# Kernel tuning notes

Hardware: AMD Instinct MI355X
Metric: run time of the kernel (lower is better)

The kernel has to match this reference:

```python
import jax, jax.numpy as jnp
import numpy as np

B, NR_BOX, D = 512, 18, 2048
NR_OBJ = NR_BOX - 2
K = 3
NUM_CLASSES = 174
NUM_CAT = 321


def setup_inputs() -> dict:
    key = jax.random.key(0)
    k1, k2, k3, k4, k5, k6 = jax.random.split(key, 6)
    obj_fea = jax.random.normal(k1, (B, NR_BOX, D), dtype=jnp.float32)
    # cooccurrence: nonnegative, sparse-ish, first (pad) column zero as in the torch code
    cooc = jax.random.uniform(k2, (NUM_CLASSES, NUM_CAT), dtype=jnp.float32)
    mask = jax.random.uniform(k3, (NUM_CLASSES, NUM_CAT)) < 0.5
    cooc = jnp.where(mask, cooc, 0.0).at[:, 0].set(0.0)
    obj_indicator = jax.random.randint(k4, (B, NR_BOX), 0, 2).astype(jnp.int32)
    obj_category = jax.random.randint(k5, (B, NR_BOX), 0, NUM_CAT).astype(jnp.int32)
    labels = jax.random.randint(k6, (B,), 0, NUM_CLASSES).astype(jnp.int32)
    return {
        'obj_fea': obj_fea,
        'cooccurrence': cooc,
        'obj_indicator': obj_indicator,
        'obj_category': obj_category,
        'labels': labels,
    }


def reference(obj_fea, cooccurrence, obj_indicator, obj_category, labels):
    Bn, nr_box, d = obj_fea.shape
    nr_obj = nr_box - 2
    ind = obj_indicator[:, 2:]          # (B, nr_obj)
    cats = obj_category[:, 2:]          # (B, nr_obj)
    ori_comp = obj_fea.mean(axis=1)     # (B, d)
    objs = obj_fea[:, 2:]               # (B, nr_obj, d), hands dropped
    label_onehot = jax.nn.one_hot(labels, NUM_CLASSES, dtype=obj_fea.dtype)  # (B, C)

    # W[i, b, j] = cooccurrence[labels[i], cats[b, j]]  (candidate weights per sample i)
    cooc_lab = cooccurrence[labels]                 # (B, NUM_CAT)
    W = cooc_lab[:, cats]                           # (B, B, nr_obj)
    eye = jnp.eye(Bn, dtype=bool)
    W = jnp.where(eye[:, :, None], 0.0, W)          # exclude own video (cand_obj[i] = 0)
    Wf = W.reshape(Bn, Bn * nr_obj)

    # softmax(log w) over nonzero support == w / sum(w); sample via categorical on log-weights
    logits = jnp.where(Wf > 0, jnp.log(jnp.where(Wf > 0, Wf, 1.0)), -jnp.inf)
    has_cand = (Wf > 0).any(axis=1) & (ind != 0).any(axis=1)  # (B,)

    rng = jax.random.key(42)
    r1, r2, r3 = jax.random.split(rng, 3)
    sel = jax.random.categorical(r1, logits, shape=(K, Bn)).T   # (B, K) flat candidate ids
    batch_idx = sel // nr_obj
    box_idx = sel % nr_obj
    sel_fea = objs[batch_idx, box_idx]              # (B, K, d)
    sel_label = label_onehot[batch_idx]             # (B, K, C)

    lam = jax.random.uniform(r2, (Bn, 1, 1), dtype=obj_fea.dtype)  # Beta(1,1)==U(0,1), one per sample
    slots = jax.random.randint(r3, (Bn, K), 0, nr_obj)
    own_fea = jnp.take_along_axis(objs, slots[:, :, None], axis=1)  # (B, K, d)

    mixed_fea = own_fea * lam + sel_fea * (1.0 - lam)
    mixed_label = label_onehot[:, None, :] * lam + sel_label * (1.0 - lam)

    # fallback path: mean of own objects + own one-hot label, repeated K times
    fb_fea = jnp.broadcast_to(objs.mean(axis=1)[:, None, :], mixed_fea.shape)
    fb_label = jnp.broadcast_to(label_onehot[:, None, :], mixed_label.shape)
    m = has_cand[:, None, None]
    mix_fea = jnp.where(m, mixed_fea, fb_fea)
    mix_label = jnp.where(m, mixed_label, fb_label)
    return ori_comp, mix_fea, mix_label
```

## Files before the change

### kernel.cpp

```cpp
#include <hip/hip_runtime.h>
#include <stdint.h>
#include <math.h>

#define NBOX 18
#define BB 512
#define DD 2048
#define NOBJ 16
#define KK 3
#define NCLS 174
#define NCAT 321
#define NQ 4
#define QCAND 2048
#define NPART 16

__host__ __device__ __forceinline__ uint32_t rotl32(uint32_t x, int d) {
  return (x << d) | (x >> (32 - d));
}

__host__ __device__ __forceinline__ void threefry2x32(uint32_t k0, uint32_t k1,
                                                      uint32_t x0, uint32_t x1,
                                                      uint32_t& o0, uint32_t& o1) {
  uint32_t ks2 = k0 ^ k1 ^ 0x1BD11BDAu;
  x0 += k0; x1 += k1;
#define TFR(r) x0 += x1; x1 = rotl32(x1, r); x1 ^= x0;
#define R4A TFR(13) TFR(15) TFR(26) TFR(6)
#define R4B TFR(17) TFR(29) TFR(16) TFR(24)
  R4A x0 += k1;  x1 += ks2 + 1u;
  R4B x0 += ks2; x1 += k0 + 2u;
  R4A x0 += k0;  x1 += k1 + 3u;
  R4B x0 += k1;  x1 += ks2 + 4u;
  R4A x0 += ks2; x1 += k0 + 5u;
#undef R4A
#undef R4B
#undef TFR
  o0 = x0; o1 = x1;
}

__device__ __forceinline__ float bits_to_unit(uint32_t bits) {
  float f = __uint_as_float((bits >> 9) | 0x3f800000u);
  return f - 1.0f;
}

__global__ __launch_bounds__(256) void sample_kernel(
    const float* __restrict__ cooc, const int* __restrict__ obj_cat,
    const int* __restrict__ labels, uint32_t r1h, uint32_t r1l,
    unsigned long long* __restrict__ part, int* __restrict__ cnts) {
  const int gb = blockIdx.x;
  const int b = gb >> 2;
  const int q = gb & 3;
  const int tid = threadIdx.x;
  const int lane = tid & 63;
  const int wid = tid >> 6;

  __shared__ unsigned short jl[QCAND];
  __shared__ float wl[QCAND];

  const int lab = labels[b];
  const float* crow = cooc + (size_t)lab * NCAT;
  const int seg = wid << 9;
  const int jbase = (q << 11) + seg;

  int cnt = 0;
#pragma unroll 1
  for (int c = 0; c < 8; ++c) {
    int j = jbase + (c << 6) + lane;
    int jb = j >> 4;
    float w = 0.0f;
    if (jb != b) w = crow[obj_cat[jb * NBOX + 2 + (j & 15)]];
    unsigned long long m = __ballot(w > 0.0f);
    if (w > 0.0f) {
      int rank = __popcll(m & ((1ull << lane) - 1ull));
      jl[seg + cnt + rank] = (unsigned short)j;
      wl[seg + cnt + rank] = w;
    }
    cnt += __popcll(m);
  }

  const uint32_t cbase0 = ((uint32_t)b) << 13;
  const uint32_t kstep = 1u << 22;
  float bw0 = 0.f, bt0 = 1.f, bw1 = 0.f, bt1 = 1.f, bw2 = 0.f, bt2 = 1.f;
  int bj0 = 0, bj1 = 0, bj2 = 0;
#pragma unroll 1
  for (int p = lane; p < cnt; p += 64) {
    uint32_t j = jl[seg + p];
    float w = wl[seg + p];
    uint32_t cc = cbase0 + j;
    uint32_t x0, x1, y0, y1, z0, z1;
    threefry2x32(r1h, r1l, 0u, cc, x0, x1);
    threefry2x32(r1h, r1l, 0u, cc + kstep, y0, y1);
    threefry2x32(r1h, r1l, 0u, cc + 2u * kstep, z0, z1);
    float t0 = -__log2f(fmaxf(bits_to_unit(x0 ^ x1), 1.1920929e-07f));
    float t1 = -__log2f(fmaxf(bits_to_unit(y0 ^ y1), 1.1920929e-07f));
    float t2 = -__log2f(fmaxf(bits_to_unit(z0 ^ z1), 1.1920929e-07f));
    if (w * bt0 > bw0 * t0) { bw0 = w; bt0 = t0; bj0 = (int)j; }
    if (w * bt1 > bw1 * t1) { bw1 = w; bt1 = t1; bj1 = (int)j; }
    if (w * bt2 > bw2 * t2) { bw2 = w; bt2 = t2; bj2 = (int)j; }
  }
#pragma unroll
  for (int mm = 1; mm < 64; mm <<= 1) {
    float ow, ot; int oj;
    ow = __shfl_xor(bw0, mm, 64); ot = __shfl_xor(bt0, mm, 64); oj = __shfl_xor(bj0, mm, 64);
    { float l = ow * bt0, r = bw0 * ot;
      if (l > r || (l == r && oj < bj0)) { bw0 = ow; bt0 = ot; bj0 = oj; } }
    ow = __shfl_xor(bw1, mm, 64); ot = __shfl_xor(bt1, mm, 64); oj = __shfl_xor(bj1, mm, 64);
    { float l = ow * bt1, r = bw1 * ot;
      if (l > r || (l == r && oj < bj1)) { bw1 = ow; bt1 = ot; bj1 = oj; } }
    ow = __shfl_xor(bw2, mm, 64); ot = __shfl_xor(bt2, mm, 64); oj = __shfl_xor(bj2, mm, 64);
    { float l = ow * bt2, r = bw2 * ot;
      if (l > r || (l == r && oj < bj2)) { bw2 = ow; bt2 = ot; bj2 = oj; } }
  }
  if (lane == 0) {
    const int pw = q * 4 + wid;
    const size_t pb = (size_t)b * KK * NPART;
    part[pb + 0 * NPART + pw] =
        ((unsigned long long)__float_as_uint(bw0 / bt0) << 32) | (uint32_t)(8192 - bj0);
    part[pb + 1 * NPART + pw] =
        ((unsigned long long)__float_as_uint(bw1 / bt1) << 32) | (uint32_t)(8192 - bj1);
    part[pb + 2 * NPART + pw] =
        ((unsigned long long)__float_as_uint(bw2 / bt2) << 32) | (uint32_t)(8192 - bj2);
    cnts[b * NPART + pw] = cnt;
  }
}

__global__ __launch_bounds__(256) void stream_mix_kernel(
    const float* __restrict__ obj_fea, const int* __restrict__ obj_ind,
    const int* __restrict__ labels,
    const unsigned long long* __restrict__ part, const int* __restrict__ cnts,
    uint32_t r2h, uint32_t r2l, uint32_t r3bh, uint32_t r3bl,
    float* __restrict__ ori, float* __restrict__ mixf, float* __restrict__ mixl) {
  const int bx = blockIdx.x;
  const int b = bx >> 1;
  const int h = bx & 1;
  const int tid = threadIdx.x;
  const int off = (h << 8) + tid;

  __shared__ int s_sel[KK];
  __shared__ int s_slots[KK];
  __shared__ float s_lam;
  __shared__ int s_hc;

  if (tid < KK) {
    const int k = tid;
    const unsigned long long* pp = part + ((size_t)b * KK + k) * NPART;
    unsigned long long best = pp[0];
#pragma unroll
    for (int p = 1; p < NPART; ++p) {
      unsigned long long v = pp[p];
      if (v > best) best = v;
    }
    s_sel[k] = 8192 - (int)(best & 0xFFFFFFFFull);
    uint32_t s0, s1;
    threefry2x32(r3bh, r3bl, 0u, (uint32_t)(b * KK + k), s0, s1);
    s_slots[k] = (int)((s0 ^ s1) & 15u);
  } else if (tid == 3) {
    int tot = 0;
#pragma unroll
    for (int p = 0; p < NPART; ++p) tot += cnts[b * NPART + p];
    int any = 0;
#pragma unroll
    for (int o = 0; o < NOBJ; ++o) any |= (obj_ind[b * NBOX + 2 + o] != 0);
    s_hc = (tot > 0) && any;
  } else if (tid == 4) {
    uint32_t c0, c1;
    threefry2x32(r2h, r2l, 0u, (uint32_t)b, c0, c1);
    s_lam = bits_to_unit(c0 ^ c1);
  }

  const float4* fea4 = (const float4*)obj_fea;
  const size_t rb = (size_t)b * NBOX * 512 + off;
  float4 v0 = fea4[rb];
  float4 v1 = fea4[rb + 512];
  float4 S = make_float4(v0.x + v1.x, v0.y + v1.y, v0.z + v1.z, v0.w + v1.w);
#pragma unroll
  for (int r = 2; r < NBOX; ++r) {
    float4 a = fea4[rb + (size_t)r * 512];
    S.x += a.x; S.y += a.y; S.z += a.z; S.w += a.w;
  }
  {
    const float is = 1.0f / 18.0f;
    ((float4*)ori)[(size_t)b * 512 + off] =
        make_float4(S.x * is, S.y * is, S.z * is, S.w * is);
  }
  float4 S16 = make_float4(S.x - v0.x - v1.x, S.y - v0.y - v1.y,
                           S.z - v0.z - v1.z, S.w - v0.w - v1.w);
  __syncthreads();

  const int hc = s_hc;
  const float l = s_lam, l1 = 1.0f - l;
  float4* mixf4 = (float4*)mixf;
  if (hc) {
#pragma unroll 1
    for (int k = 0; k < KK; ++k) {
      int s = s_sel[k];
      int bi = s >> 4, bo = s & 15, sl = s_slots[k];
      float4 a = fea4[((size_t)b * NBOX + 2 + sl) * 512 + off];
      float4 e = fea4[((size_t)bi * NBOX + 2 + bo) * 512 + off];
      float4 o;
      o.x = a.x * l + e.x * l1; o.y = a.y * l + e.y * l1;
      o.z = a.z * l + e.z * l1; o.w = a.w * l + e.w * l1;
      mixf4[((size_t)b * KK + k) * 512 + off] = o;
    }
  } else {
    const float is = 1.0f / 16.0f;
    float4 o = make_float4(S16.x * is, S16.y * is, S16.z * is, S16.w * is);
#pragma unroll
    for (int k = 0; k < KK; ++k) mixf4[((size_t)b * KK + k) * 512 + off] = o;
  }

  if (h == 0 && tid < NCLS) {
    int lb = labels[b];
#pragma unroll 1
    for (int k = 0; k < KK; ++k) {
      float val;
      if (hc) {
        int ls = labels[s_sel[k] >> 4];
        val = (tid == lb ? l : 0.0f) + (tid == ls ? l1 : 0.0f);
      } else {
        val = (tid == lb) ? 1.0f : 0.0f;
      }
      mixl[(size_t)(b * KK + k) * NCLS + tid] = val;
    }
  }
}

extern "C" void kernel_launch(void* const* d_in, const int* in_sizes, int n_in,
                              void* d_out, int out_size, void* d_ws, size_t ws_size,
                              hipStream_t stream) {
  (void)in_sizes; (void)n_in; (void)out_size; (void)ws_size;
  const float* obj_fea = (const float*)d_in[0];
  const float* cooc    = (const float*)d_in[1];
  const int* obj_ind   = (const int*)d_in[2];
  const int* obj_cat   = (const int*)d_in[3];
  const int* labels    = (const int*)d_in[4];

  float* out  = (float*)d_out;
  float* ori  = out;
  float* mixf = out + (size_t)BB * DD;
  float* mixl = mixf + (size_t)BB * KK * DD;

  char* ws = (char*)d_ws;
  unsigned long long* part = (unsigned long long*)ws;
  int* cnts = (int*)(ws + (size_t)BB * KK * NPART * 8);

  uint32_t r1h, r1l, r2h, r2l, r3h, r3l;
  threefry2x32(0u, 42u, 0u, 0u, r1h, r1l);
  threefry2x32(0u, 42u, 0u, 1u, r2h, r2l);
  threefry2x32(0u, 42u, 0u, 2u, r3h, r3l);
  uint32_t r3bh, r3bl;
  threefry2x32(r3h, r3l, 0u, 1u, r3bh, r3bl);

  hipLaunchKernelGGL(sample_kernel, dim3(BB * NQ), dim3(256), 0, stream,
                     cooc, obj_cat, labels, r1h, r1l, part, cnts);
  hipLaunchKernelGGL(stream_mix_kernel, dim3(BB * 2), dim3(256), 0, stream,
                     obj_fea, obj_ind, labels, part, cnts,
                     r2h, r2l, r3bh, r3bl, ori, mixf, mixl);
}
```

Baseline: 46.41 us.

## Fuse feature-mean streaming into sampling kernel via async global-to-LDS loads

The full obj_fea streaming (mean over 18 boxes for ori and the 16-object fallback mean) moves from the mix kernel into the sampling kernel. There it is issued as asynchronous global_load_lds transfers that overlap the threefry-based categorical sampling. The sampling grid grows from 4 to 16 slices per sample, giving 64 partial winners. The mix kernel reduces those with a wave shuffle and reads the precomputed fallback mean from workspace. This aims to hide the bandwidth-bound reduction behind the compute-bound RNG work, at the cost of extra workspace traffic and more partials to combine.

After: 52.41 us. +12.9%, slower.

```diff
diff --git a/kernel.cpp b/kernel.cpp
--- a/kernel.cpp
+++ b/kernel.cpp
@@ -9,9 +9,9 @@
 #define KK 3
 #define NCLS 174
 #define NCAT 321
-#define NQ 4
-#define QCAND 2048
-#define NPART 16
+#define NSL 16
+#define SCAND 512
+#define NPART 64
 
 __host__ __device__ __forceinline__ uint32_t rotl32(uint32_t x, int d) {
   return (x << d) | (x >> (32 - d));
@@ -41,28 +41,47 @@
   return f - 1.0f;
 }
 
-__global__ __launch_bounds__(256) void sample_kernel(
-    const float* __restrict__ cooc, const int* __restrict__ obj_cat,
-    const int* __restrict__ labels, uint32_t r1h, uint32_t r1l,
-    unsigned long long* __restrict__ part, int* __restrict__ cnts) {
+__device__ __forceinline__ void gload_lds16(const void* g, void* l) {
+  __builtin_amdgcn_global_load_lds(
+      (const __attribute__((address_space(1))) unsigned int*)g,
+      (__attribute__((address_space(3))) unsigned int*)l, 16, 0, 0);
+}
+
+__global__ __launch_bounds__(256) void sample_stream_kernel(
+    const float* __restrict__ obj_fea, const float* __restrict__ cooc,
+    const int* __restrict__ obj_cat, const int* __restrict__ labels,
+    uint32_t r1h, uint32_t r1l,
+    unsigned long long* __restrict__ part, int* __restrict__ cnts,
+    float* __restrict__ ori, float4* __restrict__ m16ws) {
   const int gb = blockIdx.x;
-  const int b = gb >> 2;
-  const int q = gb & 3;
+  const int b = gb >> 4;
+  const int o = gb & 15;
   const int tid = threadIdx.x;
   const int lane = tid & 63;
   const int wid = tid >> 6;
 
-  __shared__ unsigned short jl[QCAND];
-  __shared__ float wl[QCAND];
+  __shared__ float4 slds[NBOX * 32];
+  __shared__ unsigned short jl[SCAND];
+  __shared__ float wl[SCAND];
+
+  const int col0 = o << 5;
+  const float4* fea4 = (const float4*)obj_fea;
+  {
+    const float4* gbase = fea4 + (size_t)b * NBOX * 512 + col0;
+    for (int i = wid; i < 9; i += 4) {
+      const float4* g = gbase + (size_t)(2 * i + (lane >> 5)) * 512 + (lane & 31);
+      gload_lds16((const void*)g, (void*)((char*)slds + i * 1024));
+    }
+  }
+  __builtin_amdgcn_sched_barrier(0);
 
   const int lab = labels[b];
   const float* crow = cooc + (size_t)lab * NCAT;
-  const int seg = wid << 9;
-  const int jbase = (q << 11) + seg;
-
+  const int seg = wid << 7;
+  const int jbase = (o << 9) + seg;
   int cnt = 0;
 #pragma unroll 1
-  for (int c = 0; c < 8; ++c) {
+  for (int c = 0; c < 2; ++c) {
     int j = jbase + (c << 6) + lane;
     int jb = j >> 4;
     float w = 0.0f;
@@ -100,17 +119,17 @@
   for (int mm = 1; mm < 64; mm <<= 1) {
     float ow, ot; int oj;
     ow = __shfl_xor(bw0, mm, 64); ot = __shfl_xor(bt0, mm, 64); oj = __shfl_xor(bj0, mm, 64);
-    { float l = ow * bt0, r = bw0 * ot;
-      if (l > r || (l == r && oj < bj0)) { bw0 = ow; bt0 = ot; bj0 = oj; } }
+    { float lv = ow * bt0, rv = bw0 * ot;
+      if (lv > rv || (lv == rv && oj < bj0)) { bw0 = ow; bt0 = ot; bj0 = oj; } }
     ow = __shfl_xor(bw1, mm, 64); ot = __shfl_xor(bt1, mm, 64); oj = __shfl_xor(bj1, mm, 64);
-    { float l = ow * bt1, r = bw1 * ot;
-      if (l > r || (l == r && oj < bj1)) { bw1 = ow; bt1 = ot; bj1 = oj; } }
+    { float lv = ow * bt1, rv = bw1 * ot;
+      if (lv > rv || (lv == rv && oj < bj1)) { bw1 = ow; bt1 = ot; bj1 = oj; } }
     ow = __shfl_xor(bw2, mm, 64); ot = __shfl_xor(bt2, mm, 64); oj = __shfl_xor(bj2, mm, 64);
-    { float l = ow * bt2, r = bw2 * ot;
-      if (l > r || (l == r && oj < bj2)) { bw2 = ow; bt2 = ot; bj2 = oj; } }
+    { float lv = ow * bt2, rv = bw2 * ot;
+      if (lv > rv || (lv == rv && oj < bj2)) { bw2 = ow; bt2 = ot; bj2 = oj; } }
   }
   if (lane == 0) {
-    const int pw = q * 4 + wid;
+    const int pw = (o << 2) + wid;
     const size_t pb = (size_t)b * KK * NPART;
     part[pb + 0 * NPART + pw] =
         ((unsigned long long)__float_as_uint(bw0 / bt0) << 32) | (uint32_t)(8192 - bj0);
@@ -120,14 +139,41 @@
         ((unsigned long long)__float_as_uint(bw2 / bt2) << 32) | (uint32_t)(8192 - bj2);
     cnts[b * NPART + pw] = cnt;
   }
-}
-
-__global__ __launch_bounds__(256) void stream_mix_kernel(
+
+  __syncthreads();
+  if (wid == 0) {
+    const int col = lane & 31;
+    const int rh = lane >> 5;
+    float4 acc = make_float4(0.f, 0.f, 0.f, 0.f);
+    float4 v0 = acc, v1 = acc;
+#pragma unroll
+    for (int r = 0; r < 9; ++r) {
+      float4 t = slds[(rh * 9 + r) * 32 + col];
+      if (r == 0) v0 = t;
+      if (r == 1) v1 = t;
+      acc.x += t.x; acc.y += t.y; acc.z += t.z; acc.w += t.w;
+    }
+    float4 oth;
+    oth.x = __shfl_xor(acc.x, 32, 64); oth.y = __shfl_xor(acc.y, 32, 64);
+    oth.z = __shfl_xor(acc.z, 32, 64); oth.w = __shfl_xor(acc.w, 32, 64);
+    if (rh == 0) {
+      float4 S = make_float4(acc.x + oth.x, acc.y + oth.y, acc.z + oth.z, acc.w + oth.w);
+      const float i18 = 1.0f / 18.0f, i16 = 1.0f / 16.0f;
+      const size_t oidx = (size_t)b * 512 + col0 + col;
+      ((float4*)ori)[oidx] = make_float4(S.x * i18, S.y * i18, S.z * i18, S.w * i18);
+      m16ws[oidx] = make_float4((S.x - v0.x - v1.x) * i16, (S.y - v0.y - v1.y) * i16,
+                                (S.z - v0.z - v1.z) * i16, (S.w - v0.w - v1.w) * i16);
+    }
+  }
+}
+
+__global__ __launch_bounds__(256) void mix_kernel(
     const float* __restrict__ obj_fea, const int* __restrict__ obj_ind,
     const int* __restrict__ labels,
     const unsigned long long* __restrict__ part, const int* __restrict__ cnts,
+    const float4* __restrict__ m16ws,
     uint32_t r2h, uint32_t r2l, uint32_t r3bh, uint32_t r3bl,
-    float* __restrict__ ori, float* __restrict__ mixf, float* __restrict__ mixl) {
+    float* __restrict__ mixf, float* __restrict__ mixl) {
   const int bx = blockIdx.x;
   const int b = bx >> 1;
   const int h = bx & 1;
@@ -137,56 +183,48 @@
   __shared__ int s_sel[KK];
   __shared__ int s_slots[KK];
   __shared__ float s_lam;
-  __shared__ int s_hc;
-
-  if (tid < KK) {
-    const int k = tid;
-    const unsigned long long* pp = part + ((size_t)b * KK + k) * NPART;
-    unsigned long long best = pp[0];
-#pragma unroll
-    for (int p = 1; p < NPART; ++p) {
-      unsigned long long v = pp[p];
-      if (v > best) best = v;
-    }
-    s_sel[k] = 8192 - (int)(best & 0xFFFFFFFFull);
+  __shared__ int s_cnt;
+  __shared__ int s_any;
+
+  if (tid < 64) {
+    unsigned long long p0 = part[((size_t)b * KK + 0) * NPART + tid];
+    unsigned long long p1 = part[((size_t)b * KK + 1) * NPART + tid];
+    unsigned long long p2 = part[((size_t)b * KK + 2) * NPART + tid];
+    int ct = cnts[b * NPART + tid];
+#pragma unroll
+    for (int mm = 1; mm < 64; mm <<= 1) {
+      unsigned long long q;
+      q = __shfl_xor(p0, mm, 64); if (q > p0) p0 = q;
+      q = __shfl_xor(p1, mm, 64); if (q > p1) p1 = q;
+      q = __shfl_xor(p2, mm, 64); if (q > p2) p2 = q;
+      ct |= __shfl_xor(ct, mm, 64);
+    }
+    if (tid == 0) {
+      s_sel[0] = 8192 - (int)(p0 & 0xFFFFFFFFull);
+      s_sel[1] = 8192 - (int)(p1 & 0xFFFFFFFFull);
+      s_sel[2] = 8192 - (int)(p2 & 0xFFFFFFFFull);
+      s_cnt = ct;
+    }
+  } else if (tid < 67) {
+    const int k = tid - 64;
     uint32_t s0, s1;
     threefry2x32(r3bh, r3bl, 0u, (uint32_t)(b * KK + k), s0, s1);
     s_slots[k] = (int)((s0 ^ s1) & 15u);
-  } else if (tid == 3) {
-    int tot = 0;
-#pragma unroll
-    for (int p = 0; p < NPART; ++p) tot += cnts[b * NPART + p];
-    int any = 0;
-#pragma unroll
-    for (int o = 0; o < NOBJ; ++o) any |= (obj_ind[b * NBOX + 2 + o] != 0);
-    s_hc = (tot > 0) && any;
-  } else if (tid == 4) {
+  } else if (tid == 67) {
     uint32_t c0, c1;
     threefry2x32(r2h, r2l, 0u, (uint32_t)b, c0, c1);
     s_lam = bits_to_unit(c0 ^ c1);
-  }
-
+  } else if (tid == 68) {
+    int any = 0;
+#pragma unroll
+    for (int oo = 0; oo < NOBJ; ++oo) any |= (obj_ind[b * NBOX + 2 + oo] != 0);
+    s_any = any;
+  }
+  __syncthreads();
+
+  const int hc = (s_cnt != 0) && s_any;
+  const float l = s_lam, l1 = 1.0f - l;
   const float4* fea4 = (const float4*)obj_fea;
-  const size_t rb = (size_t)b * NBOX * 512 + off;
-  float4 v0 = fea4[rb];
-  float4 v1 = fea4[rb + 512];
-  float4 S = make_float4(v0.x + v1.x, v0.y + v1.y, v0.z + v1.z, v0.w + v1.w);
-#pragma unroll
-  for (int r = 2; r < NBOX; ++r) {
-    float4 a = fea4[rb + (size_t)r * 512];
-    S.x += a.x; S.y += a.y; S.z += a.z; S.w += a.w;
-  }
-  {
-    const float is = 1.0f / 18.0f;
-    ((float4*)ori)[(size_t)b * 512 + off] =
-        make_float4(S.x * is, S.y * is, S.z * is, S.w * is);
-  }
-  float4 S16 = make_float4(S.x - v0.x - v1.x, S.y - v0.y - v1.y,
-                           S.z - v0.z - v1.z, S.w - v0.w - v1.w);
-  __syncthreads();
-
-  const int hc = s_hc;
-  const float l = s_lam, l1 = 1.0f - l;
   float4* mixf4 = (float4*)mixf;
   if (hc) {
 #pragma unroll 1
@@ -195,16 +233,15 @@
       int bi = s >> 4, bo = s & 15, sl = s_slots[k];
       float4 a = fea4[((size_t)b * NBOX + 2 + sl) * 512 + off];
       float4 e = fea4[((size_t)bi * NBOX + 2 + bo) * 512 + off];
-      float4 o;
-      o.x = a.x * l + e.x * l1; o.y = a.y * l + e.y * l1;
-      o.z = a.z * l + e.z * l1; o.w = a.w * l + e.w * l1;
-      mixf4[((size_t)b * KK + k) * 512 + off] = o;
+      float4 ov;
+      ov.x = a.x * l + e.x * l1; ov.y = a.y * l + e.y * l1;
+      ov.z = a.z * l + e.z * l1; ov.w = a.w * l + e.w * l1;
+      mixf4[((size_t)b * KK + k) * 512 + off] = ov;
     }
   } else {
-    const float is = 1.0f / 16.0f;
-    float4 o = make_float4(S16.x * is, S16.y * is, S16.z * is, S16.w * is);
-#pragma unroll
-    for (int k = 0; k < KK; ++k) mixf4[((size_t)b * KK + k) * 512 + off] = o;
+    float4 m16 = m16ws[(size_t)b * 512 + off];
+#pragma unroll
+    for (int k = 0; k < KK; ++k) mixf4[((size_t)b * KK + k) * 512 + off] = m16;
   }
 
   if (h == 0 && tid < NCLS) {
@@ -241,6 +278,7 @@
   char* ws = (char*)d_ws;
   unsigned long long* part = (unsigned long long*)ws;
   int* cnts = (int*)(ws + (size_t)BB * KK * NPART * 8);
+  float4* m16ws = (float4*)(ws + 1024 * 1024);
 
   uint32_t r1h, r1l, r2h, r2l, r3h, r3l;
   threefry2x32(0u, 42u, 0u, 0u, r1h, r1l);
@@ -249,9 +287,10 @@
   uint32_t r3bh, r3bl;
   threefry2x32(r3h, r3l, 0u, 1u, r3bh, r3bl);
 
-  hipLaunchKernelGGL(sample_kernel, dim3(BB * NQ), dim3(256), 0, stream,
-                     cooc, obj_cat, labels, r1h, r1l, part, cnts);
-  hipLaunchKernelGGL(stream_mix_kernel, dim3(BB * 2), dim3(256), 0, stream,
-                     obj_fea, obj_ind, labels, part, cnts,
-                     r2h, r2l, r3bh, r3bl, ori, mixf, mixl);
-}
+  hipLaunchKernelGGL(sample_stream_kernel, dim3(BB * NSL), dim3(256), 0, stream,
+                     obj_fea, cooc, obj_cat, labels, r1h, r1l,
+                     part, cnts, ori, m16ws);
+  hipLaunchKernelGGL(mix_kernel, dim3(BB * 2), dim3(256), 0, stream,
+                     obj_fea, obj_ind, labels, part, cnts, m16ws,
+                     r2h, r2l, r3bh, r3bl, mixf, mixl);
+}
```
